# Optimization experiments

Hardware: AMD Instinct MI355X
Metric: run time of the kernel (lower is better)

The kernel has to match this reference:

```python
import jax, jax.numpy as jnp
import numpy as np

N = 50000
E = 800000
IN_C = 128
HID = 8
HEADS = 8
OUT_C = 16
NEG_SLOPE = 0.2


def setup_inputs() -> dict:
    key = jax.random.key(0)
    ks = jax.random.split(key, 10)
    x = jax.random.normal(ks[0], (N, IN_C), dtype=jnp.float32)
    edge_index = jax.random.randint(ks[1], (2, E), 0, N, dtype=jnp.int64)
    # layer 1: GATConv(IN_C, HID, heads=HEADS, concat=True)
    s1 = 1.0 / np.sqrt(IN_C)
    W1 = jax.random.normal(ks[2], (HEADS * HID, IN_C), dtype=jnp.float32) * s1
    att_src1 = jax.random.normal(ks[3], (HEADS, HID), dtype=jnp.float32) * 0.1
    att_dst1 = jax.random.normal(ks[4], (HEADS, HID), dtype=jnp.float32) * 0.1
    b1 = jnp.zeros((HEADS * HID,), dtype=jnp.float32)
    # layer 2: GATConv(HEADS*HID, OUT_C, heads=1, concat=False)
    s2 = 1.0 / np.sqrt(HEADS * HID)
    W2 = jax.random.normal(ks[5], (OUT_C, HEADS * HID), dtype=jnp.float32) * s2
    att_src2 = jax.random.normal(ks[6], (1, OUT_C), dtype=jnp.float32) * 0.1
    att_dst2 = jax.random.normal(ks[7], (1, OUT_C), dtype=jnp.float32) * 0.1
    b2 = jnp.zeros((OUT_C,), dtype=jnp.float32)
    return {"x": x, "edge_index": edge_index, "W1": W1, "att_src1": att_src1,
            "att_dst1": att_dst1, "b1": b1, "W2": W2, "att_src2": att_src2,
            "att_dst2": att_dst2, "b2": b2}


def _gat_conv(x, W, att_src, att_dst, bias, src, dst, concat):
    # x: [N, F_in]; W: [H*C, F_in]; att_*: [H, C]
    H, C = att_src.shape
    h = (x @ W.T).reshape(N, H, C)                       # [N, H, C]
    a_src = jnp.einsum('nhc,hc->nh', h, att_src)          # [N, H]
    a_dst = jnp.einsum('nhc,hc->nh', h, att_dst)          # [N, H]
    e = a_src[src] + a_dst[dst]                           # [Etot, H]
    e = jnp.where(e > 0, e, NEG_SLOPE * e)                # LeakyReLU(0.2)
    # segment softmax over edges grouped by destination node
    m = jax.ops.segment_max(e, dst, num_segments=N)       # [N, H]
    e = jnp.exp(e - m[dst])
    denom = jax.ops.segment_sum(e, dst, num_segments=N)   # [N, H]
    alpha = e / (denom[dst] + 1e-16)                      # [Etot, H]
    msg = alpha[:, :, None] * h[src]                      # [Etot, H, C]
    out = jax.ops.segment_sum(msg, dst, num_segments=N)   # [N, H, C]
    if concat:
        out = out.reshape(N, H * C)
    else:
        out = out.mean(axis=1)
    return out + bias


def reference(x, edge_index, W1, att_src1, att_dst1, b1, W2, att_src2, att_dst2, b2):
    # add self-loops (PyG GATConv default)
    loops = jnp.arange(N, dtype=edge_index.dtype)
    src = jnp.concatenate([edge_index[0], loops])
    dst = jnp.concatenate([edge_index[1], loops])
    h = _gat_conv(x, W1, att_src1, att_dst1, b1, src, dst, concat=True)
    h = jax.nn.elu(h)  # dropout is identity in eval mode
    return _gat_conv(h, W2, att_src2, att_dst2, b2, src, dst, concat=False)
```

## Files before the change

kernel.cpp:

```cpp
#include <hip/hip_runtime.h>
#include <hip/hip_fp16.h>
#include <math.h>

#define NN 50000
#define NE 800000
#define ETOT (NE + NN)
#define INC 128
#define F1 64
#define NH 8
#define OC 16
#define NEG 0.2f
#define BSH 7
#define NBUK 391
#define CHUNK_A 4096
#define NBLK_A ((ETOT + CHUNK_A - 1) / CHUNK_A)

__device__ __forceinline__ float leaky(float x){ return x > 0.f ? x : NEG * x; }

__device__ __forceinline__ void getsd(const int* __restrict__ ei, int e, int& s, int& d){
    if (e < NE){ s = ei[e]; d = ei[NE + e]; }
    else { s = e - NE; d = s; }
}


__global__ __launch_bounds__(256) void zero_gbcnt(int* __restrict__ gbcnt){
    int i = blockIdx.x*256 + threadIdx.x;
    if (i < NBUK) gbcnt[i] = 0;
}

__global__ __launch_bounds__(256) void bucket_hist(const int* __restrict__ ei, int* __restrict__ gbcnt){
    __shared__ int bcnt[NBUK];
    int tid = threadIdx.x;
    for (int j = tid; j < NBUK; j += 256) bcnt[j] = 0;
    __syncthreads();
    int e0 = blockIdx.x * CHUNK_A;
    int e1 = e0 + CHUNK_A; if (e1 > ETOT) e1 = ETOT;
    for (int e = e0 + tid; e < e1; e += 256){
        int d = (e < NE) ? ei[NE + e] : e - NE;
        atomicAdd(&bcnt[d >> BSH], 1);
    }
    __syncthreads();
    for (int j = tid; j < NBUK; j += 256)
        if (bcnt[j]) atomicAdd(&gbcnt[j], bcnt[j]);
}

__global__ __launch_bounds__(512) void bucket_scan(const int* __restrict__ gbcnt,
        int* __restrict__ gboff, int* __restrict__ gbcur){
    __shared__ int s[512];
    int t = threadIdx.x;
    int v = (t < NBUK) ? gbcnt[t] : 0;
    s[t] = v; __syncthreads();
    for (int off = 1; off < 512; off <<= 1){
        int u = (t >= off) ? s[t - off] : 0;
        __syncthreads();
        s[t] += u;
        __syncthreads();
    }
    if (t < NBUK){ int ex = s[t] - v; gboff[t] = ex; gbcur[t] = ex; }
    if (t == 0) gboff[NBUK] = ETOT;
}

__global__ __launch_bounds__(256) void bucket_scatter(const int* __restrict__ ei,
        int* __restrict__ gbcur, unsigned* __restrict__ packed){
    __shared__ int bcnt[NBUK];
    int tid = threadIdx.x;
    for (int j = tid; j < NBUK; j += 256) bcnt[j] = 0;
    __syncthreads();
    int e0 = blockIdx.x * CHUNK_A;
    int e1 = e0 + CHUNK_A; if (e1 > ETOT) e1 = ETOT;
    for (int e = e0 + tid; e < e1; e += 256){
        int d = (e < NE) ? ei[NE + e] : e - NE;
        atomicAdd(&bcnt[d >> BSH], 1);
    }
    __syncthreads();
    for (int j = tid; j < NBUK; j += 256){
        int c = bcnt[j];
        bcnt[j] = c ? atomicAdd(&gbcur[j], c) : 0;
    }
    __syncthreads();
    for (int e = e0 + tid; e < e1; e += 256){
        int s, d; getsd(ei, e, s, d);
        int pos = atomicAdd(&bcnt[d >> BSH], 1);
        packed[pos] = ((unsigned)s << 16) | (unsigned)d;
    }
}

__global__ __launch_bounds__(256) void bucket_finalize(const unsigned* __restrict__ packed,
        const int* __restrict__ gboff, int* __restrict__ rowstart, int* __restrict__ esrc){
    __shared__ int ldeg[1 << BSH];
    __shared__ int lcur[1 << BSH];
    __shared__ int wtot[2];
    int b = blockIdx.x, t = threadIdx.x;
    if (t < (1 << BSH)) ldeg[t] = 0;
    __syncthreads();
    int p0 = gboff[b], p1 = gboff[b+1];
    for (int i = p0 + t; i < p1; i += 256)
        atomicAdd(&ldeg[packed[i] & ((1 << BSH) - 1)], 1);
    __syncthreads();
    if (t < (1 << BSH)){
        int v = ldeg[t];
        int lane = t & 63, w = t >> 6;
        int iv = v;
        #pragma unroll
        for (int off = 1; off < 64; off <<= 1){
            int u = __shfl_up(iv, off);
            if (lane >= off) iv += u;
        }
        lcur[t] = iv;
        if (lane == 63) wtot[w] = iv;
    }
    __syncthreads();
    if (t < (1 << BSH)){
        int v = ldeg[t];
        int w = t >> 6;
        int incl = lcur[t] + (w ? wtot[0] : 0);
        int rs = p0 + incl - v;
        int n = (b << BSH) + t;
        if (n < NN) rowstart[n] = rs;
        lcur[t] = rs;
    }
    if (b == 0 && t == 0) rowstart[NN] = ETOT;
    __syncthreads();
    for (int i = p0 + t; i < p1; i += 256){
        unsigned p = packed[i];
        int pos = atomicAdd(&lcur[p & ((1 << BSH) - 1)], 1);
        esrc[pos] = (int)(p >> 16);
    }
}


__global__ __launch_bounds__(256, 4) void gemm1(const float* __restrict__ x, const float* __restrict__ W1,
        __half* __restrict__ h1h){
    __shared__ float xs[64*144];
    int tid = threadIdx.x;
    int base = blockIdx.x * 64;
    int w = tid >> 6, lane = tid & 63;
    int oL = lane >> 2, ks = lane & 3;
    int o1 = (w & 1)*32 + oL, o2 = o1 + 16;
    float4 wra[8], wrb[8];
    {
        const float4* W4 = reinterpret_cast<const float4*>(W1);
        #pragma unroll
        for (int j4 = 0; j4 < 8; ++j4){
            wra[j4] = W4[o1*32 + ks*8 + j4];
            wrb[j4] = W4[o2*32 + ks*8 + j4];
        }
    }
    {
        #pragma unroll
        for (int j = 0; j < 8; ++j){
            int f = tid + 256*j;
            int row = f >> 5, c4 = f & 31;
            int n = base + row;
            float4 v = make_float4(0.f,0.f,0.f,0.f);
            if (n < NN) v = reinterpret_cast<const float4*>(x)[n*32 + c4];
            int sk = c4 >> 3, j4 = c4 & 7;
            *(float4*)(&xs[row*144 + sk*36 + j4*4]) = v;
        }
    }
    __syncthreads();
    int rbase = (w >> 1) * 32;
    for (int r = 0; r < 32; ++r){
        int row = rbase + r;
        const float* xb = &xs[row*144 + ks*36];
        float acc1 = 0.f, acc2 = 0.f;
        #pragma unroll
        for (int j4 = 0; j4 < 8; ++j4){
            float4 xv = *(const float4*)(xb + j4*4);
            acc1 = fmaf(xv.x, wra[j4].x, acc1);
            acc2 = fmaf(xv.x, wrb[j4].x, acc2);
            acc1 = fmaf(xv.y, wra[j4].y, acc1);
            acc2 = fmaf(xv.y, wrb[j4].y, acc2);
            acc1 = fmaf(xv.z, wra[j4].z, acc1);
            acc2 = fmaf(xv.z, wrb[j4].z, acc2);
            acc1 = fmaf(xv.w, wra[j4].w, acc1);
            acc2 = fmaf(xv.w, wrb[j4].w, acc2);
        }
        acc1 += __shfl_xor(acc1, 1); acc1 += __shfl_xor(acc1, 2);
        acc2 += __shfl_xor(acc2, 1); acc2 += __shfl_xor(acc2, 2);
        int node = base + row;
        if (ks == 0 && node < NN){
            h1h[node*64 + o1] = __float2half(acc1);
            h1h[node*64 + o2] = __float2half(acc2);
        }
    }
}

__global__ __launch_bounds__(256, 4) void gemm2(const float* __restrict__ out1, const float* __restrict__ W2,
        __half* __restrict__ h2h){
    __shared__ float xs[64*80];
    int tid = threadIdx.x;
    int base = blockIdx.x * 64;
    int w = tid >> 6, lane = tid & 63;
    int o = lane >> 2, ks = lane & 3;
    float4 wr[4];
    {
        const float4* W4 = reinterpret_cast<const float4*>(W2);
        #pragma unroll
        for (int j4 = 0; j4 < 4; ++j4)
            wr[j4] = W4[o*16 + ks*4 + j4];
    }
    {
        #pragma unroll
        for (int j = 0; j < 4; ++j){
            int f = tid + 256*j;
            int row = f >> 4, c4 = f & 15;
            int n = base + row;
            float4 v = make_float4(0.f,0.f,0.f,0.f);
            if (n < NN) v = reinterpret_cast<const float4*>(out1)[n*16 + c4];
            v.x = v.x > 0.f ? v.x : __expf(v.x) - 1.f;
            v.y = v.y > 0.f ? v.y : __expf(v.y) - 1.f;
            v.z = v.z > 0.f ? v.z : __expf(v.z) - 1.f;
            v.w = v.w > 0.f ? v.w : __expf(v.w) - 1.f;
            int sk = c4 >> 2, j4 = c4 & 3;
            *(float4*)(&xs[row*80 + sk*20 + j4*4]) = v;
        }
    }
    __syncthreads();
    for (int r = 0; r < 16; ++r){
        int row = w*16 + r;
        const float* xb = &xs[row*80 + ks*20];
        float acc = 0.f;
        #pragma unroll
        for (int j4 = 0; j4 < 4; ++j4){
            float4 xv = *(const float4*)(xb + j4*4);
            acc = fmaf(xv.x, wr[j4].x, acc);
            acc = fmaf(xv.y, wr[j4].y, acc);
            acc = fmaf(xv.z, wr[j4].z, acc);
            acc = fmaf(xv.w, wr[j4].w, acc);
        }
        acc += __shfl_xor(acc, 1); acc += __shfl_xor(acc, 2);
        int node = base + row;
        if (ks == 0 && node < NN)
            h2h[node*16 + o] = __float2half(acc);
    }
}


__global__ __launch_bounds__(256) void att1(const __half* __restrict__ h1h,
        const float* __restrict__ att_s, const float* __restrict__ att_d,
        float* __restrict__ a_src, float* __restrict__ a_dst){
    int idx = blockIdx.x*256 + threadIdx.x;
    if (idx >= NN*NH) return;
    int n = idx >> 3, h = idx & 7;
    float4 raw = reinterpret_cast<const float4*>(h1h)[n*8 + h];
    const __half2* hp = (const __half2*)&raw;
    float ds_ = 0.f, dd_ = 0.f;
    #pragma unroll
    for (int q = 0; q < 4; ++q){
        float2 f = __half22float2(hp[q]);
        ds_ = fmaf(f.x, att_s[h*8 + 2*q],     ds_);
        ds_ = fmaf(f.y, att_s[h*8 + 2*q + 1], ds_);
        dd_ = fmaf(f.x, att_d[h*8 + 2*q],     dd_);
        dd_ = fmaf(f.y, att_d[h*8 + 2*q + 1], dd_);
    }
    a_src[idx] = ds_;
    a_dst[idx] = dd_;
}

__global__ __launch_bounds__(256) void att2(const __half* __restrict__ h2h,
        const float* __restrict__ att_s, const float* __restrict__ att_d,
        float* __restrict__ a_src, float* __restrict__ a_dst){
    int n = blockIdx.x*256 + threadIdx.x;
    if (n >= NN) return;
    float4 r0 = reinterpret_cast<const float4*>(h2h)[n*2];
    float4 r1 = reinterpret_cast<const float4*>(h2h)[n*2 + 1];
    const __half2* hp0 = (const __half2*)&r0;
    const __half2* hp1 = (const __half2*)&r1;
    float ds_ = 0.f, dd_ = 0.f;
    #pragma unroll
    for (int q = 0; q < 4; ++q){
        float2 f = __half22float2(hp0[q]);
        ds_ = fmaf(f.x, att_s[2*q],   ds_); ds_ = fmaf(f.y, att_s[2*q+1], ds_);
        dd_ = fmaf(f.x, att_d[2*q],   dd_); dd_ = fmaf(f.y, att_d[2*q+1], dd_);
    }
    #pragma unroll
    for (int q = 0; q < 4; ++q){
        float2 f = __half22float2(hp1[q]);
        ds_ = fmaf(f.x, att_s[8+2*q], ds_); ds_ = fmaf(f.y, att_s[8+2*q+1], ds_);
        dd_ = fmaf(f.x, att_d[8+2*q], dd_); dd_ = fmaf(f.y, att_d[8+2*q+1], dd_);
    }
    a_src[n] = ds_;
    a_dst[n] = dd_;
}


__global__ __launch_bounds__(256) void layer1_node(const int* __restrict__ rowstart,
        const int* __restrict__ esrc, const float* __restrict__ a_src,
        const float* __restrict__ a_dst, const __half* __restrict__ h1h,
        const float* __restrict__ b1, float* __restrict__ out1){
    int wid = __builtin_amdgcn_readfirstlane((blockIdx.x*256 + threadIdx.x) >> 6);
    int lane = threadIdx.x & 63;
    if (wid >= NN) return;
    int n = wid;
    int h = lane >> 3;
    int r0 = rowstart[n], r1 = rowstart[n+1];
    float ad = a_dst[n*8 + h];
    float den0 = 0.f, acc0 = 0.f, den1 = 0.f, acc1 = 0.f;
    float den2 = 0.f, acc2 = 0.f, den3 = 0.f, acc3 = 0.f;
    float den4 = 0.f, acc4 = 0.f, den5 = 0.f, acc5 = 0.f;
    float den6 = 0.f, acc6 = 0.f, den7 = 0.f, acc7 = 0.f;
    int i = r0;
    for (; i + 7 < r1; i += 8){
        int s0 = esrc[i],   s1 = esrc[i+1], s2 = esrc[i+2], s3 = esrc[i+3];
        int s4 = esrc[i+4], s5 = esrc[i+5], s6 = esrc[i+6], s7 = esrc[i+7];
        float e0 = leaky(a_src[s0*8 + h] + ad);
        float e1 = leaky(a_src[s1*8 + h] + ad);
        float e2 = leaky(a_src[s2*8 + h] + ad);
        float e3 = leaky(a_src[s3*8 + h] + ad);
        float e4 = leaky(a_src[s4*8 + h] + ad);
        float e5 = leaky(a_src[s5*8 + h] + ad);
        float e6 = leaky(a_src[s6*8 + h] + ad);
        float e7 = leaky(a_src[s7*8 + h] + ad);
        float hv0 = __half2float(h1h[s0*64 + lane]);
        float hv1 = __half2float(h1h[s1*64 + lane]);
        float hv2 = __half2float(h1h[s2*64 + lane]);
        float hv3 = __half2float(h1h[s3*64 + lane]);
        float hv4 = __half2float(h1h[s4*64 + lane]);
        float hv5 = __half2float(h1h[s5*64 + lane]);
        float hv6 = __half2float(h1h[s6*64 + lane]);
        float hv7 = __half2float(h1h[s7*64 + lane]);
        float p0 = __expf(e0), p1 = __expf(e1), p2 = __expf(e2), p3 = __expf(e3);
        float p4 = __expf(e4), p5 = __expf(e5), p6 = __expf(e6), p7 = __expf(e7);
        den0 += p0; acc0 = fmaf(p0, hv0, acc0);
        den1 += p1; acc1 = fmaf(p1, hv1, acc1);
        den2 += p2; acc2 = fmaf(p2, hv2, acc2);
        den3 += p3; acc3 = fmaf(p3, hv3, acc3);
        den4 += p4; acc4 = fmaf(p4, hv4, acc4);
        den5 += p5; acc5 = fmaf(p5, hv5, acc5);
        den6 += p6; acc6 = fmaf(p6, hv6, acc6);
        den7 += p7; acc7 = fmaf(p7, hv7, acc7);
    }
    for (; i + 3 < r1; i += 4){
        int s0 = esrc[i], s1 = esrc[i+1], s2 = esrc[i+2], s3 = esrc[i+3];
        float e0 = leaky(a_src[s0*8 + h] + ad);
        float e1 = leaky(a_src[s1*8 + h] + ad);
        float e2 = leaky(a_src[s2*8 + h] + ad);
        float e3 = leaky(a_src[s3*8 + h] + ad);
        float hv0 = __half2float(h1h[s0*64 + lane]);
        float hv1 = __half2float(h1h[s1*64 + lane]);
        float hv2 = __half2float(h1h[s2*64 + lane]);
        float hv3 = __half2float(h1h[s3*64 + lane]);
        float p0 = __expf(e0), p1 = __expf(e1), p2 = __expf(e2), p3 = __expf(e3);
        den0 += p0; acc0 = fmaf(p0, hv0, acc0);
        den1 += p1; acc1 = fmaf(p1, hv1, acc1);
        den2 += p2; acc2 = fmaf(p2, hv2, acc2);
        den3 += p3; acc3 = fmaf(p3, hv3, acc3);
    }
    for (; i < r1; ++i){
        int s = esrc[i];
        float p = __expf(leaky(a_src[s*8 + h] + ad));
        den0 += p; acc0 = fmaf(p, __half2float(h1h[s*64 + lane]), acc0);
    }
    float den = ((den0 + den1) + (den2 + den3)) + ((den4 + den5) + (den6 + den7));
    float acc = ((acc0 + acc1) + (acc2 + acc3)) + ((acc4 + acc5) + (acc6 + acc7));
    out1[n*64 + lane] = acc/(den + 1e-16f) + b1[lane];
}

__global__ __launch_bounds__(256) void layer2_node(const int* __restrict__ rowstart,
        const int* __restrict__ esrc, const float* __restrict__ a_src,
        const float* __restrict__ a_dst, const __half* __restrict__ h2h,
        const float* __restrict__ b2, float* __restrict__ out){
    int wid = __builtin_amdgcn_readfirstlane((blockIdx.x*256 + threadIdx.x) >> 6);
    int lane = threadIdx.x & 63;
    if (wid >= NN) return;
    int n = wid;
    int slot = lane >> 4, c = lane & 15;
    int r0 = rowstart[n], r1 = rowstart[n+1];
    float ad = a_dst[n];
    float den0 = 0.f, acc0 = 0.f, den1 = 0.f, acc1 = 0.f;
    float den2 = 0.f, acc2 = 0.f, den3 = 0.f, acc3 = 0.f;
    int i = r0 + slot;
    for (; i + 12 < r1; i += 16){
        int s0 = esrc[i], s1 = esrc[i+4], s2 = esrc[i+8], s3 = esrc[i+12];
        float p0 = __expf(leaky(a_src[s0] + ad));
        float p1 = __expf(leaky(a_src[s1] + ad));
        float p2 = __expf(leaky(a_src[s2] + ad));
        float p3 = __expf(leaky(a_src[s3] + ad));
        float hv0 = __half2float(h2h[s0*16 + c]);
        float hv1 = __half2float(h2h[s1*16 + c]);
        float hv2 = __half2float(h2h[s2*16 + c]);
        float hv3 = __half2float(h2h[s3*16 + c]);
        den0 += p0; acc0 = fmaf(p0, hv0, acc0);
        den1 += p1; acc1 = fmaf(p1, hv1, acc1);
        den2 += p2; acc2 = fmaf(p2, hv2, acc2);
        den3 += p3; acc3 = fmaf(p3, hv3, acc3);
    }
    for (; i < r1; i += 4){
        int s = esrc[i];
        float p = __expf(leaky(a_src[s] + ad));
        den0 += p; acc0 = fmaf(p, __half2float(h2h[s*16 + c]), acc0);
    }
    float den = (den0 + den1) + (den2 + den3);
    float acc = (acc0 + acc1) + (acc2 + acc3);
    den += __shfl_xor(den, 16); den += __shfl_xor(den, 32);
    acc += __shfl_xor(acc, 16); acc += __shfl_xor(acc, 32);
    if (slot == 0) out[n*16 + c] = acc/(den + 1e-16f) + b2[c];
}

extern "C" void kernel_launch(void* const* d_in, const int* in_sizes, int n_in,
                              void* d_out, int out_size, void* d_ws, size_t ws_size,
                              hipStream_t stream){
    const float* x    = (const float*)d_in[0];
    const int*   ei   = (const int*)d_in[1];
    const float* W1   = (const float*)d_in[2];
    const float* as1w = (const float*)d_in[3];
    const float* ad1w = (const float*)d_in[4];
    const float* b1   = (const float*)d_in[5];
    const float* W2   = (const float*)d_in[6];
    const float* as2w = (const float*)d_in[7];
    const float* ad2w = (const float*)d_in[8];
    const float* b2   = (const float*)d_in[9];
    float* out = (float*)d_out;

    float* ws = (float*)d_ws;
    __half* h1h     = (__half*)ws;
    float* out1     = ws + (size_t)32*NN;
    int*   rowstart = (int*)(ws + (size_t)96*NN);
    int*   gbcnt    = rowstart + NN + 1;
    int*   gboff    = gbcnt + NBUK;
    int*   gbcur    = gboff + NBUK + 1;
    unsigned* packed= (unsigned*)(gbcur + NBUK);
    int*   esrc     = (int*)(packed + ETOT);
    float* a_src1 = out;
    float* a_dst1 = out + (size_t)8*NN;
    __half* h2h   = h1h;
    float* a_src2 = ws + (size_t)8*NN;
    float* a_dst2 = a_src2 + NN;

    hipLaunchKernelGGL(zero_gbcnt,      dim3(2), dim3(256), 0, stream, gbcnt);
    hipLaunchKernelGGL(bucket_hist,     dim3(NBLK_A), dim3(256), 0, stream, ei, gbcnt);
    hipLaunchKernelGGL(bucket_scan,     dim3(1), dim3(512), 0, stream, gbcnt, gboff, gbcur);
    hipLaunchKernelGGL(bucket_scatter,  dim3(NBLK_A), dim3(256), 0, stream, ei, gbcur, packed);
    hipLaunchKernelGGL(bucket_finalize, dim3(NBUK), dim3(256), 0, stream, packed, gboff, rowstart, esrc);

    hipLaunchKernelGGL(gemm1, dim3((NN + 63)/64), dim3(256), 0, stream, x, W1, h1h);
    hipLaunchKernelGGL(att1,  dim3((NN*NH + 255)/256), dim3(256), 0, stream, h1h, as1w, ad1w, a_src1, a_dst1);
    hipLaunchKernelGGL(layer1_node, dim3((NN*64 + 255)/256), dim3(256), 0, stream,
                       rowstart, esrc, a_src1, a_dst1, h1h, b1, out1);
    hipLaunchKernelGGL(gemm2, dim3((NN + 63)/64), dim3(256), 0, stream, out1, W2, h2h);
    hipLaunchKernelGGL(att2,  dim3((NN + 255)/256), dim3(256), 0, stream, h2h, as2w, ad2w, a_src2, a_dst2);
    hipLaunchKernelGGL(layer2_node, dim3((NN*64 + 255)/256), dim3(256), 0, stream,
                       rowstart, esrc, a_src2, a_dst2, h2h, b2, out);
}
```

Baseline: 135.1 us.

## Fuse attention logits into GEMMs and co-schedule bucket scatter with gemm1

Computes the per-head attention logits a_src/a_dst directly in the gemm1/gemm2 epilogues with lane shuffles, which removes the separate att1/att2 kernels and their re-read of the fp16 features. The bucket scatter blocks and the gemm1 blocks now share one grid, so the two independent jobs overlap and one launch is saved. In exchange the logits come from fp32 accumulators rather than fp16-rounded values, the combined kernel uses the larger shared-memory footprint for every block, and it now carries launch_bounds(256,4).

```diff
diff --git a/kernel.cpp b/kernel.cpp
--- a/kernel.cpp
+++ b/kernel.cpp
@@ -14,6 +14,7 @@
 #define NBUK 391
 #define CHUNK_A 4096
 #define NBLK_A ((ETOT + CHUNK_A - 1) / CHUNK_A)
+#define NBLK_G1 ((NN + 63) / 64)
 
 __device__ __forceinline__ float leaky(float x){ return x > 0.f ? x : NEG * x; }
 
@@ -60,80 +61,37 @@
     if (t == 0) gboff[NBUK] = ETOT;
 }
 
-__global__ __launch_bounds__(256) void bucket_scatter(const int* __restrict__ ei,
-        int* __restrict__ gbcur, unsigned* __restrict__ packed){
+__global__ __launch_bounds__(256, 4) void scatter_gemm1(const int* __restrict__ ei,
+        int* __restrict__ gbcur, unsigned* __restrict__ packed,
+        const float* __restrict__ x, const float* __restrict__ W1,
+        const float* __restrict__ att_s, const float* __restrict__ att_d,
+        __half* __restrict__ h1h, float* __restrict__ a_src, float* __restrict__ a_dst){
     __shared__ int bcnt[NBUK];
-    int tid = threadIdx.x;
-    for (int j = tid; j < NBUK; j += 256) bcnt[j] = 0;
-    __syncthreads();
-    int e0 = blockIdx.x * CHUNK_A;
-    int e1 = e0 + CHUNK_A; if (e1 > ETOT) e1 = ETOT;
-    for (int e = e0 + tid; e < e1; e += 256){
-        int d = (e < NE) ? ei[NE + e] : e - NE;
-        atomicAdd(&bcnt[d >> BSH], 1);
-    }
-    __syncthreads();
-    for (int j = tid; j < NBUK; j += 256){
-        int c = bcnt[j];
-        bcnt[j] = c ? atomicAdd(&gbcur[j], c) : 0;
-    }
-    __syncthreads();
-    for (int e = e0 + tid; e < e1; e += 256){
-        int s, d; getsd(ei, e, s, d);
-        int pos = atomicAdd(&bcnt[d >> BSH], 1);
-        packed[pos] = ((unsigned)s << 16) | (unsigned)d;
-    }
-}
-
-__global__ __launch_bounds__(256) void bucket_finalize(const unsigned* __restrict__ packed,
-        const int* __restrict__ gboff, int* __restrict__ rowstart, int* __restrict__ esrc){
-    __shared__ int ldeg[1 << BSH];
-    __shared__ int lcur[1 << BSH];
-    __shared__ int wtot[2];
-    int b = blockIdx.x, t = threadIdx.x;
-    if (t < (1 << BSH)) ldeg[t] = 0;
-    __syncthreads();
-    int p0 = gboff[b], p1 = gboff[b+1];
-    for (int i = p0 + t; i < p1; i += 256)
-        atomicAdd(&ldeg[packed[i] & ((1 << BSH) - 1)], 1);
-    __syncthreads();
-    if (t < (1 << BSH)){
-        int v = ldeg[t];
-        int lane = t & 63, w = t >> 6;
-        int iv = v;
-        #pragma unroll
-        for (int off = 1; off < 64; off <<= 1){
-            int u = __shfl_up(iv, off);
-            if (lane >= off) iv += u;
-        }
-        lcur[t] = iv;
-        if (lane == 63) wtot[w] = iv;
-    }
-    __syncthreads();
-    if (t < (1 << BSH)){
-        int v = ldeg[t];
-        int w = t >> 6;
-        int incl = lcur[t] + (w ? wtot[0] : 0);
-        int rs = p0 + incl - v;
-        int n = (b << BSH) + t;
-        if (n < NN) rowstart[n] = rs;
-        lcur[t] = rs;
-    }
-    if (b == 0 && t == 0) rowstart[NN] = ETOT;
-    __syncthreads();
-    for (int i = p0 + t; i < p1; i += 256){
-        unsigned p = packed[i];
-        int pos = atomicAdd(&lcur[p & ((1 << BSH) - 1)], 1);
-        esrc[pos] = (int)(p >> 16);
-    }
-}
-
-
-__global__ __launch_bounds__(256, 4) void gemm1(const float* __restrict__ x, const float* __restrict__ W1,
-        __half* __restrict__ h1h){
     __shared__ float xs[64*144];
     int tid = threadIdx.x;
-    int base = blockIdx.x * 64;
+    if (blockIdx.x < NBLK_A){
+        for (int j = tid; j < NBUK; j += 256) bcnt[j] = 0;
+        __syncthreads();
+        int e0 = blockIdx.x * CHUNK_A;
+        int e1 = e0 + CHUNK_A; if (e1 > ETOT) e1 = ETOT;
+        for (int e = e0 + tid; e < e1; e += 256){
+            int d = (e < NE) ? ei[NE + e] : e - NE;
+            atomicAdd(&bcnt[d >> BSH], 1);
+        }
+        __syncthreads();
+        for (int j = tid; j < NBUK; j += 256){
+            int c = bcnt[j];
+            bcnt[j] = c ? atomicAdd(&gbcur[j], c) : 0;
+        }
+        __syncthreads();
+        for (int e = e0 + tid; e < e1; e += 256){
+            int s, d; getsd(ei, e, s, d);
+            int pos = atomicAdd(&bcnt[d >> BSH], 1);
+            packed[pos] = ((unsigned)s << 16) | (unsigned)d;
+        }
+        return;
+    }
+    int base = (blockIdx.x - NBLK_A) * 64;
     int w = tid >> 6, lane = tid & 63;
     int oL = lane >> 2, ks = lane & 3;
     int o1 = (w & 1)*32 + oL, o2 = o1 + 16;
@@ -146,6 +104,8 @@
             wrb[j4] = W4[o2*32 + ks*8 + j4];
         }
     }
+    float as_o1 = att_s[o1], as_o2 = att_s[o2];
+    float ad_o1 = att_d[o1], ad_o2 = att_d[o2];
     {
         #pragma unroll
         for (int j = 0; j < 8; ++j){
@@ -160,6 +120,7 @@
     }
     __syncthreads();
     int rbase = (w >> 1) * 32;
+    int hA = (w & 1)*4 + (oL >> 3);
     for (int r = 0; r < 32; ++r){
         int row = rbase + r;
         const float* xb = &xs[row*144 + ks*36];
@@ -179,15 +140,74 @@
         acc1 += __shfl_xor(acc1, 1); acc1 += __shfl_xor(acc1, 2);
         acc2 += __shfl_xor(acc2, 1); acc2 += __shfl_xor(acc2, 2);
         int node = base + row;
-        if (ks == 0 && node < NN){
-            h1h[node*64 + o1] = __float2half(acc1);
-            h1h[node*64 + o2] = __float2half(acc2);
-        }
-    }
-}
+        float p1s = acc1 * as_o1, p2s = acc2 * as_o2;
+        float p1d = acc1 * ad_o1, p2d = acc2 * ad_o2;
+        p1s += __shfl_xor(p1s, 4); p1s += __shfl_xor(p1s, 8); p1s += __shfl_xor(p1s, 16);
+        p2s += __shfl_xor(p2s, 4); p2s += __shfl_xor(p2s, 8); p2s += __shfl_xor(p2s, 16);
+        p1d += __shfl_xor(p1d, 4); p1d += __shfl_xor(p1d, 8); p1d += __shfl_xor(p1d, 16);
+        p2d += __shfl_xor(p2d, 4); p2d += __shfl_xor(p2d, 8); p2d += __shfl_xor(p2d, 16);
+        if (node < NN){
+            if (ks == 0){
+                h1h[node*64 + o1] = __float2half(acc1);
+                h1h[node*64 + o2] = __float2half(acc2);
+                if ((oL & 7) == 0){
+                    a_src[node*8 + hA]     = p1s;
+                    a_dst[node*8 + hA]     = p1d;
+                    a_src[node*8 + hA + 2] = p2s;
+                    a_dst[node*8 + hA + 2] = p2d;
+                }
+            }
+        }
+    }
+}
+
+__global__ __launch_bounds__(256) void bucket_finalize(const unsigned* __restrict__ packed,
+        const int* __restrict__ gboff, int* __restrict__ rowstart, int* __restrict__ esrc){
+    __shared__ int ldeg[1 << BSH];
+    __shared__ int lcur[1 << BSH];
+    __shared__ int wtot[2];
+    int b = blockIdx.x, t = threadIdx.x;
+    if (t < (1 << BSH)) ldeg[t] = 0;
+    __syncthreads();
+    int p0 = gboff[b], p1 = gboff[b+1];
+    for (int i = p0 + t; i < p1; i += 256)
+        atomicAdd(&ldeg[packed[i] & ((1 << BSH) - 1)], 1);
+    __syncthreads();
+    if (t < (1 << BSH)){
+        int v = ldeg[t];
+        int lane = t & 63, w = t >> 6;
+        int iv = v;
+        #pragma unroll
+        for (int off = 1; off < 64; off <<= 1){
+            int u = __shfl_up(iv, off);
+            if (lane >= off) iv += u;
+        }
+        lcur[t] = iv;
+        if (lane == 63) wtot[w] = iv;
+    }
+    __syncthreads();
+    if (t < (1 << BSH)){
+        int v = ldeg[t];
+        int w = t >> 6;
+        int incl = lcur[t] + (w ? wtot[0] : 0);
+        int rs = p0 + incl - v;
+        int n = (b << BSH) + t;
+        if (n < NN) rowstart[n] = rs;
+        lcur[t] = rs;
+    }
+    if (b == 0 && t == 0) rowstart[NN] = ETOT;
+    __syncthreads();
+    for (int i = p0 + t; i < p1; i += 256){
+        unsigned p = packed[i];
+        int pos = atomicAdd(&lcur[p & ((1 << BSH) - 1)], 1);
+        esrc[pos] = (int)(p >> 16);
+    }
+}
+
 
 __global__ __launch_bounds__(256, 4) void gemm2(const float* __restrict__ out1, const float* __restrict__ W2,
-        __half* __restrict__ h2h){
+        const float* __restrict__ att_s, const float* __restrict__ att_d,
+        __half* __restrict__ h2h, float* __restrict__ a_src, float* __restrict__ a_dst){
     __shared__ float xs[64*80];
     int tid = threadIdx.x;
     int base = blockIdx.x * 64;
@@ -200,6 +220,7 @@
         for (int j4 = 0; j4 < 4; ++j4)
             wr[j4] = W4[o*16 + ks*4 + j4];
     }
+    float as_o = att_s[o], ad_o = att_d[o];
     {
         #pragma unroll
         for (int j = 0; j < 4; ++j){
@@ -231,57 +252,16 @@
         }
         acc += __shfl_xor(acc, 1); acc += __shfl_xor(acc, 2);
         int node = base + row;
-        if (ks == 0 && node < NN)
-            h2h[node*16 + o] = __float2half(acc);
-    }
-}
-
-
-__global__ __launch_bounds__(256) void att1(const __half* __restrict__ h1h,
-        const float* __restrict__ att_s, const float* __restrict__ att_d,
-        float* __restrict__ a_src, float* __restrict__ a_dst){
-    int idx = blockIdx.x*256 + threadIdx.x;
-    if (idx >= NN*NH) return;
-    int n = idx >> 3, h = idx & 7;
-    float4 raw = reinterpret_cast<const float4*>(h1h)[n*8 + h];
-    const __half2* hp = (const __half2*)&raw;
-    float ds_ = 0.f, dd_ = 0.f;
-    #pragma unroll
-    for (int q = 0; q < 4; ++q){
-        float2 f = __half22float2(hp[q]);
-        ds_ = fmaf(f.x, att_s[h*8 + 2*q],     ds_);
-        ds_ = fmaf(f.y, att_s[h*8 + 2*q + 1], ds_);
-        dd_ = fmaf(f.x, att_d[h*8 + 2*q],     dd_);
-        dd_ = fmaf(f.y, att_d[h*8 + 2*q + 1], dd_);
-    }
-    a_src[idx] = ds_;
-    a_dst[idx] = dd_;
-}
-
-__global__ __launch_bounds__(256) void att2(const __half* __restrict__ h2h,
-        const float* __restrict__ att_s, const float* __restrict__ att_d,
-        float* __restrict__ a_src, float* __restrict__ a_dst){
-    int n = blockIdx.x*256 + threadIdx.x;
-    if (n >= NN) return;
-    float4 r0 = reinterpret_cast<const float4*>(h2h)[n*2];
-    float4 r1 = reinterpret_cast<const float4*>(h2h)[n*2 + 1];
-    const __half2* hp0 = (const __half2*)&r0;
-    const __half2* hp1 = (const __half2*)&r1;
-    float ds_ = 0.f, dd_ = 0.f;
-    #pragma unroll
-    for (int q = 0; q < 4; ++q){
-        float2 f = __half22float2(hp0[q]);
-        ds_ = fmaf(f.x, att_s[2*q],   ds_); ds_ = fmaf(f.y, att_s[2*q+1], ds_);
-        dd_ = fmaf(f.x, att_d[2*q],   dd_); dd_ = fmaf(f.y, att_d[2*q+1], dd_);
-    }
-    #pragma unroll
-    for (int q = 0; q < 4; ++q){
-        float2 f = __half22float2(hp1[q]);
-        ds_ = fmaf(f.x, att_s[8+2*q], ds_); ds_ = fmaf(f.y, att_s[8+2*q+1], ds_);
-        dd_ = fmaf(f.x, att_d[8+2*q], dd_); dd_ = fmaf(f.y, att_d[8+2*q+1], dd_);
-    }
-    a_src[n] = ds_;
-    a_dst[n] = dd_;
+        float ps = acc * as_o, pd = acc * ad_o;
+        ps += __shfl_xor(ps, 4); ps += __shfl_xor(ps, 8);
+        ps += __shfl_xor(ps, 16); ps += __shfl_xor(ps, 32);
+        pd += __shfl_xor(pd, 4); pd += __shfl_xor(pd, 8);
+        pd += __shfl_xor(pd, 16); pd += __shfl_xor(pd, 32);
+        if (node < NN){
+            if (ks == 0) h2h[node*16 + o] = __float2half(acc);
+            if (lane == 0){ a_src[node] = ps; a_dst[node] = pd; }
+        }
+    }
 }
 
 
@@ -431,15 +411,13 @@
     hipLaunchKernelGGL(zero_gbcnt,      dim3(2), dim3(256), 0, stream, gbcnt);
     hipLaunchKernelGGL(bucket_hist,     dim3(NBLK_A), dim3(256), 0, stream, ei, gbcnt);
     hipLaunchKernelGGL(bucket_scan,     dim3(1), dim3(512), 0, stream, gbcnt, gboff, gbcur);
-    hipLaunchKernelGGL(bucket_scatter,  dim3(NBLK_A), dim3(256), 0, stream, ei, gbcur, packed);
+    hipLaunchKernelGGL(scatter_gemm1,   dim3(NBLK_A + NBLK_G1), dim3(256), 0, stream,
+                       ei, gbcur, packed, x, W1, as1w, ad1w, h1h, a_src1, a_dst1);
     hipLaunchKernelGGL(bucket_finalize, dim3(NBUK), dim3(256), 0, stream, packed, gboff, rowstart, esrc);
 
-    hipLaunchKernelGGL(gemm1, dim3((NN + 63)/64), dim3(256), 0, stream, x, W1, h1h);
-    hipLaunchKernelGGL(att1,  dim3((NN*NH + 255)/256), dim3(256), 0, stream, h1h, as1w, ad1w, a_src1, a_dst1);
     hipLaunchKernelGGL(layer1_node, dim3((NN*64 + 255)/256), dim3(256), 0, stream,
                        rowstart, esrc, a_src1, a_dst1, h1h, b1, out1);
-    hipLaunchKernelGGL(gemm2, dim3((NN + 63)/64), dim3(256), 0, stream, out1, W2, h2h);
-    hipLaunchKernelGGL(att2,  dim3((NN + 255)/256), dim3(256), 0, stream, h2h, as2w, ad2w, a_src2, a_dst2);
+    hipLaunchKernelGGL(gemm2, dim3((NN + 63)/64), dim3(256), 0, stream, out1, W2, as2w, ad2w, h2h, a_src2, a_dst2);
     hipLaunchKernelGGL(layer2_node, dim3((NN*64 + 255)/256), dim3(256), 0, stream,
                        rowstart, esrc, a_src2, a_dst2, h2h, b2, out);
 }
```

After: 137.7 us. Within noise of the previous version (+2.0%).
